# Performance work log

Hardware: AMD Instinct MI355X
Metric: run time of the kernel (lower is better)

Reference implementation:

```python
import jax, jax.numpy as jnp
import numpy as np

K, STRIDE, PAD, DIL = 3, 1, 1, 1
EPS = 1e-20


def kernel_channels(x):
    # x: [B, C, H, W] -> [B, C, K*K, H', W'] (row-major kernel ordering, as torch F.unfold)
    xp = jnp.pad(x, ((0, 0), (0, 0), (PAD, PAD), (PAD, PAD)))
    Hp, Wp = xp.shape[2], xp.shape[3]
    Ho = (Hp - DIL * (K - 1) - 1) // STRIDE + 1
    Wo = (Wp - DIL * (K - 1) - 1) // STRIDE + 1
    patches = [xp[:, :, i * DIL:i * DIL + (Ho - 1) * STRIDE + 1:STRIDE,
                       j * DIL:j * DIL + (Wo - 1) * STRIDE + 1:STRIDE]
               for i in range(K) for j in range(K)]
    return jnp.stack(patches, axis=2)


def setup_inputs() -> dict:
    key = jax.random.key(0)
    ks = jax.random.split(key, 8)
    B, Cin, Cout, H, W = 4, 32, 32, 256, 256
    d = jax.random.normal(ks[0], (B, Cin, H, W), jnp.float32)
    cd = jax.random.uniform(ks[1], (B, Cin, H, W), jnp.float32)          # confidences in [0,1)
    s = jax.random.uniform(ks[2], (B, Cin, H, W), jnp.float32)           # unused in forward (API compat)
    cs = jax.random.uniform(ks[3], (B, Cin, H, W), jnp.float32)          # unused in forward (API compat)
    s_prod_roll = jax.random.uniform(ks[4], (B, Cin, K * K, H, W), jnp.float32)
    channel_weight = jax.random.normal(ks[5], (Cout, Cin, 1, 1), jnp.float32)
    spatial_weight = jax.random.normal(ks[6], (Cin, 1, K * K, 1, 1), jnp.float32)
    bias = jax.random.normal(ks[7], (1, Cout, 1, 1), jnp.float32) * 0.01
    return {"d": d, "cd": cd, "s": s, "cs": cs, "s_prod_roll": s_prod_roll,
            "channel_weight": channel_weight, "spatial_weight": spatial_weight, "bias": bias}


def reference(d, cd, s, cs, s_prod_roll, channel_weight, spatial_weight, bias):
    # EnforcePos: weights are passed through softplus before use
    sw = jax.nn.softplus(spatial_weight)[:, 0, :, 0, 0]   # [Cin, K*K]
    cw = jax.nn.softplus(channel_weight)[:, :, 0, 0]      # [Cout, Cin]

    d_roll = kernel_channels(d)                            # [B, Cin, K*K, H, W]
    cd_roll = kernel_channels(cd)
    cd_prop = cd_roll * s_prod_roll

    # conv3d with groups=Cin, depth kernel K*K == per-channel weighted sum over neighbor axis
    nom = jnp.einsum('bckhw,ck->bchw', cd_prop * d_roll, sw)
    denom = jnp.einsum('bckhw,ck->bchw', cd_prop, sw)
    d_spatial = nom / (denom + EPS)
    cd_spatial = denom / jnp.sum(sw)

    # 1x1 conv2d, groups=1 == channel mixing
    nom2 = jnp.einsum('bchw,oc->bohw', cd_spatial * d_spatial, cw)
    denom2 = jnp.einsum('bchw,oc->bohw', cd_spatial, cw)
    d_out = nom2 / (denom2 + EPS) + bias
    cd_out = denom2 / jnp.sum(cw) / (STRIDE * STRIDE)
    return d_out, cd_out
```

## Files before the change

### kernel.cpp

```cpp
#include <hip/hip_runtime.h>

#define EPS 1e-20f
typedef float f4 __attribute__((ext_vector_type(4)));

__global__ void prep_weights(const float* __restrict__ channel_weight,
                             const float* __restrict__ spatial_weight,
                             float* __restrict__ ws) {
    __shared__ float red[256];
    int tid = threadIdx.x;
    float local_sw = 0.f, local_cw = 0.f;
    for (int i = tid; i < 288; i += 256) {
        float x = spatial_weight[i];
        float v = fmaxf(x, 0.f) + log1pf(expf(-fabsf(x)));
        ws[i] = v;
        local_sw += v;
    }
    for (int i = tid; i < 1024; i += 256) {
        float x = channel_weight[i];
        float v = fmaxf(x, 0.f) + log1pf(expf(-fabsf(x)));
        int o = i >> 5, c = i & 31;
        ws[288 + c * 32 + o] = v;
        local_cw += v;
    }
    red[tid] = local_sw;
    __syncthreads();
    for (int s = 128; s > 0; s >>= 1) {
        if (tid < s) red[tid] += red[tid + s];
        __syncthreads();
    }
    if (tid == 0) ws[1312] = 1.0f / red[0];
    __syncthreads();
    red[tid] = local_cw;
    __syncthreads();
    for (int s = 128; s > 0; s >>= 1) {
        if (tid < s) red[tid] += red[tid + s];
        __syncthreads();
    }
    if (tid == 0) ws[1313] = 1.0f / red[0];
}

__global__ __launch_bounds__(256) void fused8(
    const float* __restrict__ d,
    const float* __restrict__ cd,
    const float* __restrict__ sp,
    const float* __restrict__ wsbuf,
    const float* __restrict__ bias,
    float* __restrict__ out)
{
    __shared__ float lt[32 * 64];
    __shared__ float lc[32 * 64];
    __shared__ float lcw[1024];

    const int plane = 65536;

    int bid = blockIdx.x;
    bid = (bid & 7) * 512 + (bid >> 3);

    const int qt = bid & 3;
    const int h  = (bid >> 2) & 255;
    const int b  = bid >> 10;

    const int tid = threadIdx.x;

    #pragma unroll
    for (int i = 0; i < 4; ++i) lcw[i * 256 + tid] = wsbuf[288 + i * 256 + tid];

    const int w    = tid >> 6;
    const int cs   = (tid >> 4) & 3;
    const int pq   = tid & 15;
    const int col0 = qt * 64 + pq * 4;
    const float inv_sum_sw = wsbuf[1312];
    const bool rowv0 = (h >= 1), rowv2 = (h <= 254);

    #pragma unroll 1
    for (int iter = 0; iter < 2; ++iter) {
        const int c  = w * 8 + iter * 4 + cs;
        const int bc = b * 32 + c;
        const float* __restrict__ dC  = d  + (size_t)bc * plane;
        const float* __restrict__ cdC = cd + (size_t)bc * plane;
        const float* __restrict__ spC = sp + (size_t)bc * 9 * plane + h * 256;

        f4 spv[9];
        #pragma unroll
        for (int k = 0; k < 9; ++k)
            spv[k] = __builtin_nontemporal_load((const f4*)(spC + (size_t)k * plane + col0));

        float dr[3][6], cr[3][6];
        #pragma unroll
        for (int i = 0; i < 3; ++i) {
            const int hh = h + i - 1;
            const int hc = min(max(hh, 0), 255);
            const float* __restrict__ drow = dC  + hc * 256;
            const float* __restrict__ crow = cdC + hc * 256;
            f4 dv = *(const f4*)(drow + col0);
            f4 cv = *(const f4*)(crow + col0);
            dr[i][1] = dv[0]; dr[i][2] = dv[1]; dr[i][3] = dv[2]; dr[i][4] = dv[3];
            cr[i][1] = cv[0]; cr[i][2] = cv[1]; cr[i][3] = cv[2]; cr[i][4] = cv[3];
            dr[i][0] = drow[max(col0 - 1, 0)];
            cr[i][0] = crow[max(col0 - 1, 0)];
            dr[i][5] = drow[min(col0 + 4, 255)];
            cr[i][5] = crow[min(col0 + 4, 255)];
        }

        float swk[9];
        #pragma unroll
        for (int k = 0; k < 9; ++k) swk[k] = wsbuf[c * 9 + k];

        float nom[4] = {0.f, 0.f, 0.f, 0.f}, den[4] = {0.f, 0.f, 0.f, 0.f};
        #pragma unroll
        for (int i = 0; i < 3; ++i) {
            const bool rv = (i == 0) ? rowv0 : ((i == 2) ? rowv2 : true);
            #pragma unroll
            for (int j = 0; j < 3; ++j) {
                const int k = i * 3 + j;
                const float s = swk[k];
                #pragma unroll
                for (int p = 0; p < 4; ++p) {
                    const int ww = col0 + p + j - 1;
                    const bool valid = rv && ((unsigned)ww < 256u);
                    const float cdp = valid ? cr[i][p + j] * spv[k][p] : 0.f;
                    nom[p] = fmaf(cdp * dr[i][p + j], s, nom[p]);
                    den[p] = fmaf(cdp, s, den[p]);
                }
            }
        }

        f4 tv, cv4;
        #pragma unroll
        for (int p = 0; p < 4; ++p) {
            tv[p]  = nom[p] * inv_sum_sw;
            cv4[p] = den[p] * inv_sum_sw;
        }
        *(f4*)&lt[c * 64 + pq * 4] = tv;
        *(f4*)&lc[c * 64 + pq * 4] = cv4;
    }

    __syncthreads();

    const int og = tid >> 4;
    const int o0 = og * 2;

    float n2[2][4], d2[2][4];
    #pragma unroll
    for (int oi = 0; oi < 2; ++oi)
        #pragma unroll
        for (int j = 0; j < 4; ++j) { n2[oi][j] = 0.f; d2[oi][j] = 0.f; }

    for (int cc = 0; cc < 32; ++cc) {
        const f4 tq = *(const f4*)&lt[cc * 64 + pq * 4];
        const f4 cq = *(const f4*)&lc[cc * 64 + pq * 4];
        const float cw0 = lcw[cc * 32 + o0];
        const float cw1 = lcw[cc * 32 + o0 + 1];
        #pragma unroll
        for (int j = 0; j < 4; ++j) {
            n2[0][j] = fmaf(tq[j], cw0, n2[0][j]);
            d2[0][j] = fmaf(cq[j], cw0, d2[0][j]);
            n2[1][j] = fmaf(tq[j], cw1, n2[1][j]);
            d2[1][j] = fmaf(cq[j], cw1, d2[1][j]);
        }
    }

    const float inv_sum_cw = wsbuf[1313];

    #pragma unroll
    for (int oi = 0; oi < 2; ++oi) {
        const float bo = bias[o0 + oi];
        f4 dv, cv;
        #pragma unroll
        for (int j = 0; j < 4; ++j) {
            dv[j] = n2[oi][j] / (d2[oi][j] + EPS) + bo;
            cv[j] = d2[oi][j] * inv_sum_cw;
        }
        const size_t po = (size_t)(b * 32 + o0 + oi) * plane + h * 256 + col0;
        *(f4*)(out + po)           = dv;
        *(f4*)(out + 8388608 + po) = cv;
    }
}

extern "C" void kernel_launch(void* const* d_in, const int* in_sizes, int n_in,
                              void* d_out, int out_size, void* d_ws, size_t ws_size,
                              hipStream_t stream) {
    const float* d    = (const float*)d_in[0];
    const float* cd   = (const float*)d_in[1];
    const float* sp   = (const float*)d_in[4];
    const float* cwt  = (const float*)d_in[5];
    const float* swt  = (const float*)d_in[6];
    const float* bias = (const float*)d_in[7];
    float* out = (float*)d_out;
    float* ws  = (float*)d_ws;

    prep_weights<<<1, 256, 0, stream>>>(cwt, swt, ws);
    fused8<<<4096, 256, 0, stream>>>(d, cd, sp, ws, bias, out);
}
```

Before: 105.1 us.

## Process full image rows per block with 8 output channels per thread

Each block now handles a full 256-column row for all 32 channels instead of a 64-column quarter row, so the grid shrinks from 4096 to 1024 blocks. The depthwise stage loops over 8 channel iterations per thread, and the channel-mixing stage computes 8 output channels per thread using vectorized weight and bias loads. This raises per-thread reuse of staged intermediates and cuts redundant weight loads per block. In exchange, LDS use grows to about 68 KB per block, which lowers occupancy, and register pressure in the mixing stage goes up.

```diff
diff --git a/kernel.cpp b/kernel.cpp
--- a/kernel.cpp
+++ b/kernel.cpp
@@ -39,7 +39,7 @@
     if (tid == 0) ws[1313] = 1.0f / red[0];
 }
 
-__global__ __launch_bounds__(256) void fused8(
+__global__ __launch_bounds__(256) void fused12(
     const float* __restrict__ d,
     const float* __restrict__ cd,
     const float* __restrict__ sp,
@@ -47,18 +47,17 @@
     const float* __restrict__ bias,
     float* __restrict__ out)
 {
-    __shared__ float lt[32 * 64];
-    __shared__ float lc[32 * 64];
+    __shared__ float lt[32 * 256];
+    __shared__ float lc[32 * 256];
     __shared__ float lcw[1024];
 
     const int plane = 65536;
 
     int bid = blockIdx.x;
-    bid = (bid & 7) * 512 + (bid >> 3);
+    bid = (bid & 7) * 128 + (bid >> 3);
 
-    const int qt = bid & 3;
-    const int h  = (bid >> 2) & 255;
-    const int b  = bid >> 10;
+    const int h = bid & 255;
+    const int b = bid >> 8;
 
     const int tid = threadIdx.x;
 
@@ -66,15 +65,14 @@
     for (int i = 0; i < 4; ++i) lcw[i * 256 + tid] = wsbuf[288 + i * 256 + tid];
 
     const int w    = tid >> 6;
-    const int cs   = (tid >> 4) & 3;
-    const int pq   = tid & 15;
-    const int col0 = qt * 64 + pq * 4;
+    const int pq   = tid & 63;
+    const int col0 = pq * 4;
     const float inv_sum_sw = wsbuf[1312];
     const bool rowv0 = (h >= 1), rowv2 = (h <= 254);
 
     #pragma unroll 1
-    for (int iter = 0; iter < 2; ++iter) {
-        const int c  = w * 8 + iter * 4 + cs;
+    for (int iter = 0; iter < 8; ++iter) {
+        const int c  = iter * 4 + w;
         const int bc = b * 32 + c;
         const float* __restrict__ dC  = d  + (size_t)bc * plane;
         const float* __restrict__ cdC = cd + (size_t)bc * plane;
@@ -131,40 +129,44 @@
             tv[p]  = nom[p] * inv_sum_sw;
             cv4[p] = den[p] * inv_sum_sw;
         }
-        *(f4*)&lt[c * 64 + pq * 4] = tv;
-        *(f4*)&lc[c * 64 + pq * 4] = cv4;
+        *(f4*)&lt[c * 256 + pq * 4] = tv;
+        *(f4*)&lc[c * 256 + pq * 4] = cv4;
     }
 
     __syncthreads();
 
-    const int og = tid >> 4;
-    const int o0 = og * 2;
+    const int og = tid >> 6;
+    const int o0 = og * 8;
 
-    float n2[2][4], d2[2][4];
+    float n2[8][4], d2[8][4];
     #pragma unroll
-    for (int oi = 0; oi < 2; ++oi)
+    for (int oi = 0; oi < 8; ++oi)
         #pragma unroll
         for (int j = 0; j < 4; ++j) { n2[oi][j] = 0.f; d2[oi][j] = 0.f; }
 
     for (int cc = 0; cc < 32; ++cc) {
-        const f4 tq = *(const f4*)&lt[cc * 64 + pq * 4];
-        const f4 cq = *(const f4*)&lc[cc * 64 + pq * 4];
-        const float cw0 = lcw[cc * 32 + o0];
-        const float cw1 = lcw[cc * 32 + o0 + 1];
+        const f4 tq = *(const f4*)&lt[cc * 256 + pq * 4];
+        const f4 cq = *(const f4*)&lc[cc * 256 + pq * 4];
+        const f4 cwA = *(const f4*)&lcw[cc * 32 + o0];
+        const f4 cwB = *(const f4*)&lcw[cc * 32 + o0 + 4];
         #pragma unroll
-        for (int j = 0; j < 4; ++j) {
-            n2[0][j] = fmaf(tq[j], cw0, n2[0][j]);
-            d2[0][j] = fmaf(cq[j], cw0, d2[0][j]);
-            n2[1][j] = fmaf(tq[j], cw1, n2[1][j]);
-            d2[1][j] = fmaf(cq[j], cw1, d2[1][j]);
-        }
+        for (int oi = 0; oi < 4; ++oi)
+            #pragma unroll
+            for (int j = 0; j < 4; ++j) {
+                n2[oi][j]     = fmaf(tq[j], cwA[oi], n2[oi][j]);
+                d2[oi][j]     = fmaf(cq[j], cwA[oi], d2[oi][j]);
+                n2[4 + oi][j] = fmaf(tq[j], cwB[oi], n2[4 + oi][j]);
+                d2[4 + oi][j] = fmaf(cq[j], cwB[oi], d2[4 + oi][j]);
+            }
     }
 
     const float inv_sum_cw = wsbuf[1313];
+    const f4 bA = *(const f4*)&bias[o0];
+    const f4 bB = *(const f4*)&bias[o0 + 4];
 
     #pragma unroll
-    for (int oi = 0; oi < 2; ++oi) {
-        const float bo = bias[o0 + oi];
+    for (int oi = 0; oi < 8; ++oi) {
+        const float bo = (oi < 4) ? bA[oi & 3] : bB[oi & 3];
         f4 dv, cv;
         #pragma unroll
         for (int j = 0; j < 4; ++j) {
@@ -190,5 +192,5 @@
     float* ws  = (float*)d_ws;
 
     prep_weights<<<1, 256, 0, stream>>>(cwt, swt, ws);
-    fused8<<<4096, 256, 0, stream>>>(d, cd, sp, ws, bias, out);
+    fused12<<<1024, 256, 0, stream>>>(d, cd, sp, ws, bias, out);
 }
```

After: 95.73 us. 8.9% less time.
